# Kernel optimization log

Measured on AMD Instinct MI355X. Metric: run time of the kernel, lower is better.

## Reference

```python
import jax, jax.numpy as jnp
from jax import lax
import numpy as np

NUM_HEADS = 8
ALPHA = 4.0  # spikingjelly default Sigmoid surrogate alpha
TAU = 2.0
BN_EPS = 1e-5

@jax.custom_vjp
def spike(x):
    # Heaviside(v - v_th) with sigmoid surrogate gradient
    return (x >= 0).astype(x.dtype)

def _spike_fwd(x):
    return spike(x), x

def _spike_bwd(x, g):
    sg = jax.nn.sigmoid(ALPHA * x)
    return (g * ALPHA * sg * (1.0 - sg),)

spike.defvjp(_spike_fwd, _spike_bwd)

def lif(x_seq, v_threshold=1.0):
    """Multi-step LIF, tau=2, hard reset to v_reset=0, detach_reset=True.
    x_seq: (T, ...) -> spikes (T, ...)."""
    def step(v, xt):
        h = v + (xt - v) / TAU
        s = spike(h - v_threshold)
        v_next = h * (1.0 - lax.stop_gradient(s))  # detach_reset hard reset
        return v_next, s
    _, s_seq = lax.scan(step, jnp.zeros_like(x_seq[0]), x_seq)
    return s_seq

def bn1d(x, gamma, beta, mean, var):
    # x: (T,B,C,N), normalize over channel dim C (eval-mode BatchNorm1d)
    inv = gamma / jnp.sqrt(var + BN_EPS)
    return x * inv[:, None] + (beta - mean * inv)[:, None]

def setup_inputs() -> dict:
    key = jax.random.key(0)
    ks = jax.random.split(key, 8)
    T, B, C, H, W = 4, 16, 384, 32, 32
    N = H * W
    Dh = C // NUM_HEADS
    x = jax.random.normal(ks[0], (T, B, C, H, W), dtype=jnp.float32)
    attn_k = jax.random.randint(ks[1], (T, B, NUM_HEADS, Dh, N), 0, 2).astype(jnp.bool_)
    attn_v = jax.random.randint(ks[2], (T, B, NUM_HEADS, Dh, N), 0, 2).astype(jnp.bool_)
    wq = jax.random.normal(ks[3], (C, C), dtype=jnp.float32) * 0.02
    wp = jax.random.normal(ks[4], (C, C), dtype=jnp.float32) * 0.02
    bp = jnp.zeros((C,), dtype=jnp.float32)
    return {
        'x': x, 'attn_k': attn_k, 'attn_v': attn_v,
        'wq': wq,
        'q_gamma': jnp.ones((C,), jnp.float32), 'q_beta': jnp.zeros((C,), jnp.float32),
        'q_mean': jnp.zeros((C,), jnp.float32), 'q_var': jnp.ones((C,), jnp.float32),
        'wp': wp, 'bp': bp,
        'p_gamma': jnp.ones((C,), jnp.float32), 'p_beta': jnp.zeros((C,), jnp.float32),
        'p_mean': jnp.zeros((C,), jnp.float32), 'p_var': jnp.ones((C,), jnp.float32),
    }

def reference(x, attn_k, attn_v, wq, q_gamma, q_beta, q_mean, q_var,
              wp, bp, p_gamma, p_beta, p_mean, p_var):
    T, B, C, H, W = x.shape
    N = H * W
    Dh = C // NUM_HEADS
    xs = lif(x).reshape(T, B, C, N)                      # shortcut_lif + flatten(3)
    q = jnp.einsum('oc,tbcn->tbon', wq, xs)              # q_conv (1x1, no bias)
    q = bn1d(q, q_gamma, q_beta, q_mean, q_var)          # q_bn
    q = lif(q)                                           # q_lif
    q = q.reshape(T, B, NUM_HEADS, Dh, N)
    kv = jnp.logical_and(attn_k, attn_v).astype(q.dtype) # attn_k & attn_v
    out = (q * kv).reshape(T, B, C, N)                   # elementwise 'attention'
    out = jnp.einsum('oc,tbcn->tbon', wp, out) + bp[:, None]  # proj_conv (bias)
    out = bn1d(out, p_gamma, p_beta, p_mean, p_var)      # proj_bn
    return out.reshape(T, B, C, H, W)
```

## Files before the change

kernel.cpp:

```cpp
#include <hip/hip_runtime.h>
#include <cstdint>

#define CN (384*1024)
#define BCN (16*CN)
#define EPS 1e-5f

typedef float f32x2 __attribute__((ext_vector_type(2)));
typedef float f32x4 __attribute__((ext_vector_type(4)));

#define WPT_OFF   0u
#define WQB_OFF   589824u
#define QINV_OFF  1179648u
#define QOFF_OFF  (QINV_OFF + 1536u)
#define PINV_OFF  (QINV_OFF + 3072u)
#define POFF_OFF  (QINV_OFF + 4608u)
#define C0_OFF    (QINV_OFF + 6144u)
#define LCNT2_OFF 1187840u
#define ROWMAX_OFF 1253376u
#define MAXQ_OFF  1254912u
#define XM_OFF    1310720u
#define XMT_OFF   4456448u
#define LISTS2_OFF 7602176u
#define ABND_OFF  10747904u
#define MST_OFF   XM_OFF

__global__ __launch_bounds__(256) void k01_lif_prep(const float* __restrict__ x,
                                                    const float* __restrict__ wq,
                                                    const float* __restrict__ wp,
                                                    const float* __restrict__ qg,
                                                    const float* __restrict__ qb,
                                                    const float* __restrict__ qm,
                                                    const float* __restrict__ qv,
                                                    const float* __restrict__ pg,
                                                    const float* __restrict__ pb,
                                                    const float* __restrict__ pm,
                                                    const float* __restrict__ pv,
                                                    const float* __restrict__ bp,
                                                    unsigned long long* __restrict__ xm,
                                                    char* __restrict__ ws) {
    if (blockIdx.x < 1536) {
        const int wv   = threadIdx.x >> 6;
        const int lane = threadIdx.x & 63;
        const int pid  = blockIdx.x * 4 + wv;
        const int b = pid / 384, c = pid % 384;
        const float* xp = x + (size_t)b * CN + (size_t)c * 1024 + lane;
        float v[16];
        #pragma unroll
        for (int g = 0; g < 16; ++g) v[g] = 0.f;
        #pragma unroll
        for (int t = 0; t < 4; ++t) {
            float xv[16];
            #pragma unroll
            for (int g = 0; g < 16; ++g)
                xv[g] = xp[(size_t)t * BCN + g * 64];
            #pragma unroll
            for (int g = 0; g < 16; ++g) {
                float h = v[g] + (xv[g] - v[g]) * 0.5f;
                bool s = (h >= 1.0f);
                unsigned long long m = __ballot(s);
                v[g] = s ? 0.f : h;
                if (lane == 0) xm[(((size_t)t * 16 + b) * 16 + g) * 384 + c] = m;
            }
        }
        return;
    }
    int bid = blockIdx.x - 1536;
    if (bid < 576) {
        int i = bid * 256 + threadIdx.x;
        int c = i / 384, o = i % 384;
        ((float*)(ws + WPT_OFF))[c * 384 + o] = wp[o * 384 + c];
    } else if (bid < 1154) {
        int j = (bid - 576) * 256 + threadIdx.x;
        if (j >= 147840) return;
        int r = j / 384, o = j % 384;
        unsigned short v = 0;
        if (r < 384) {
            unsigned u = __float_as_uint(wq[o * 384 + r]);
            v = (unsigned short)((u + 0x7fffu + ((u >> 16) & 1u)) >> 16);
        }
        ((unsigned short*)(ws + WQB_OFF))[j] = v;
    } else if (bid == 1154) {
        __shared__ float smi[256], smo[256];
        float mi = 0.f, mo = 0.f;
        for (int i = threadIdx.x; i < 384; i += 256) {
            float qi = qg[i] / sqrtf(qv[i] + EPS);
            ((float*)(ws + QINV_OFF))[i] = qi;
            float qov = qb[i] - qm[i] * qi;
            ((float*)(ws + QOFF_OFF))[i] = qov;
            float pi = pg[i] / sqrtf(pv[i] + EPS);
            float po = pb[i] - pm[i] * pi;
            ((float*)(ws + PINV_OFF))[i] = pi;
            ((float*)(ws + POFF_OFF))[i] = po;
            ((float*)(ws + C0_OFF))[i] = bp[i] * pi + po;
            mi = fmaxf(mi, fabsf(qi));
            mo = fmaxf(mo, fabsf(qov));
        }
        smi[threadIdx.x] = mi; smo[threadIdx.x] = mo;
        __syncthreads();
        for (int s = 128; s > 0; s >>= 1) {
            if (threadIdx.x < s) {
                smi[threadIdx.x] = fmaxf(smi[threadIdx.x], smi[threadIdx.x + s]);
                smo[threadIdx.x] = fmaxf(smo[threadIdx.x], smo[threadIdx.x + s]);
            }
            __syncthreads();
        }
        if (threadIdx.x == 0) {
            ((float*)(ws + MAXQ_OFF))[0] = smi[0];
            ((float*)(ws + MAXQ_OFF))[1] = smo[0];
        }
    } else {
        __shared__ float sm[256];
        int rblk = bid - 1155;
        int row = rblk * 64 + (threadIdx.x >> 2);
        int qd  = threadIdx.x & 3;
        float m = 0.f;
        for (int o = qd * 96; o < qd * 96 + 96; ++o) {
            unsigned u = __float_as_uint(wq[(size_t)o * 384 + row]);
            unsigned bbits = (u + 0x7fffu + ((u >> 16) & 1u)) >> 16;
            m = fmaxf(m, __uint_as_float((bbits & 0x7fffu) << 16));
        }
        sm[threadIdx.x] = m;
        __syncthreads();
        if (qd == 0) {
            float r0 = fmaxf(fmaxf(sm[threadIdx.x], sm[threadIdx.x + 1]),
                             fmaxf(sm[threadIdx.x + 2], sm[threadIdx.x + 3]));
            ((float*)(ws + ROWMAX_OFF))[row] = r0;
        }
    }
}

__global__ __launch_bounds__(256) void k1bc(const unsigned long long* __restrict__ xm,
                                            const float* __restrict__ rowmaxp,
                                            const float* __restrict__ maxqp,
                                            unsigned long long* __restrict__ xmT,
                                            unsigned short* __restrict__ lists2,
                                            unsigned char* __restrict__ lcnt2,
                                            unsigned char* __restrict__ abnd) {
    int wid  = (blockIdx.x * 256 + threadIdx.x) >> 6;
    int lane = threadIdx.x & 63;
    int g  = wid & 15;
    int tb = wid >> 4;
    unsigned long long T[6];
    #pragma unroll
    for (int cg = 0; cg < 6; ++cg) {
        unsigned long long W = xm[((size_t)tb * 16 + g) * 384 + cg * 64 + lane];
        unsigned long long colw = 0ull;
        #pragma unroll
        for (int k = 0; k < 64; ++k) {
            unsigned long long bk = __ballot((W >> k) & 1ull);
            if (lane == k) colw = bk;
        }
        T[cg] = colw;
    }
    const int n   = g * 64 + lane;
    const size_t col = ((size_t)tb << 10) + n;
    #pragma unroll
    for (int cg = 0; cg < 6; ++cg) xmT[col * 6 + cg] = T[cg];
    const int blockid = (tb & 15) * 64 + (n >> 4);
    const int un = (n & 15) * 4 + (tb >> 4);
    unsigned short* lp = lists2 + ((size_t)blockid * 64 + un) * 24;
    int k = 0;
    float S = 0.f;
    #pragma unroll
    for (int cg = 0; cg < 6; ++cg) {
        unsigned long long m = T[cg];
        while (m) {
            int j = __builtin_ctzll(m);
            m &= m - 1;
            S += rowmaxp[cg * 64 + j];
            if (k < 24) lp[k] = (unsigned short)((cg * 64 + j) * 3);
            ++k;
        }
    }
    int kk = k > 24 ? 24 : k;
    for (int i = kk; i < 24; ++i) lp[i] = 1152;
    lcnt2[(size_t)blockid * 64 + un] =
        (k > 24) ? 0xFF : (unsigned char)((k + 7) >> 3);
    float A = maxqp[0] * S + maxqp[1];
    int aq = (int)ceilf(A * 64.f);
    abnd[(size_t)blockid * 64 + un] = (unsigned char)(aq > 255 ? 255 : (aq < 0 ? 0 : aq));
}

#define BLO(w) __uint_as_float((w) << 16)
#define BHI(w) __uint_as_float((w) & 0xFFFF0000u)
#define PK(w)  ((f32x2){BLO(w), BHI(w)})
#define RL(v, l) ((unsigned)__builtin_amdgcn_readlane((int)(v), (l)))

#define GROW8(W0, W1, W2, W3) do {                                                \
    uint3 d0_ = *(const uint3*)(wqc + ((size_t)((W0) & 0xffffu) << 8) + voff);    \
    uint3 d1_ = *(const uint3*)(wqc + ((size_t)((W0) >> 16) << 8) + voff);        \
    uint3 d2_ = *(const uint3*)(wqc + ((size_t)((W1) & 0xffffu) << 8) + voff);    \
    uint3 d3_ = *(const uint3*)(wqc + ((size_t)((W1) >> 16) << 8) + voff);        \
    uint3 d4_ = *(const uint3*)(wqc + ((size_t)((W2) & 0xffffu) << 8) + voff);    \
    uint3 d5_ = *(const uint3*)(wqc + ((size_t)((W2) >> 16) << 8) + voff);        \
    uint3 d6_ = *(const uint3*)(wqc + ((size_t)((W3) & 0xffffu) << 8) + voff);    \
    uint3 d7_ = *(const uint3*)(wqc + ((size_t)((W3) >> 16) << 8) + voff);        \
    s0 += ((PK(d0_.x) + PK(d1_.x)) + (PK(d2_.x) + PK(d3_.x)))                     \
        + ((PK(d4_.x) + PK(d5_.x)) + (PK(d6_.x) + PK(d7_.x)));                    \
    s1 += ((PK(d0_.y) + PK(d1_.y)) + (PK(d2_.y) + PK(d3_.y)))                     \
        + ((PK(d4_.y) + PK(d5_.y)) + (PK(d6_.y) + PK(d7_.y)));                    \
    s2 += ((PK(d0_.z) + PK(d1_.z)) + (PK(d2_.z) + PK(d3_.z)))                     \
        + ((PK(d4_.z) + PK(d5_.z)) + (PK(d6_.z) + PK(d7_.z)));                    \
} while (0)

__global__ __launch_bounds__(512) void k2_qpath(const char* __restrict__ wqc,
                                                const float* __restrict__ qinv_,
                                                const float* __restrict__ qoff_,
                                                const unsigned short* __restrict__ lists2,
                                                const unsigned char* __restrict__ lcnt2,
                                                const unsigned char* __restrict__ abnd,
                                                const unsigned long long* __restrict__ xmT,
                                                const unsigned char* __restrict__ ak,
                                                const unsigned char* __restrict__ av,
                                                const float* __restrict__ c0,
                                                unsigned long long* __restrict__ msT,
                                                float* __restrict__ out) {
    const int tid  = threadIdx.x;
    const int lane = tid & 63;
    const int w    = tid >> 6;
    const int nt   = blockIdx.x & 63;
    const int b    = blockIdx.x >> 6;
    const int voff = lane * 12;

    const char* lb = (const char*)lists2 + (size_t)blockIdx.x * 3072 + lane * 48;
    const uint4 L0 = *(const uint4*)lb;
    const uint4 L1 = *(const uint4*)(lb + 16);
    const uint4 L2 = *(const uint4*)(lb + 32);
    const unsigned lcv = *(const unsigned*)((const char*)lcnt2
                          + (size_t)blockIdx.x * 64 + (lane & 15) * 4);
    const unsigned abv = *(const unsigned*)((const char*)abnd
                          + (size_t)blockIdx.x * 64 + (lane & 15) * 4);

    float qi[6], qo[6];
    #pragma unroll
    for (int e = 0; e < 6; ++e) {
        qi[e] = qinv_[lane * 6 + e];
        qo[e] = qoff_[lane * 6 + e];
    }

    #pragma unroll
    for (int i = 0; i < 2; ++i) {
        const int nl = w * 2 + i;
        const int n  = nt * 16 + nl;
        const unsigned abw = RL(abv, nl);
        float hb = 0.f;
        bool skip = true;
        #pragma unroll
        for (int t = 0; t < 4; ++t) {
            float A = (float)((abw >> (8 * t)) & 0xffu) * 0.015625f + 0.015625f;
            hb = 0.5f * (hb + A);
            skip = skip && (hb < 1.0f);
        }
        if (skip) {
            if (lane < 6) {
                #pragma unroll
                for (int t = 0; t < 4; ++t)
                    msT[(size_t)(((t * 16 + b) << 10) + n) * 6 + lane] = 0ull;
            }
            continue;
        }
        const unsigned lcw = RL(lcv, nl);
        float v[6] = {0.f, 0.f, 0.f, 0.f, 0.f, 0.f};
        #pragma unroll
        for (int t = 0; t < 4; ++t) {
            const int un = nl * 4 + t;
            const unsigned r_ = (lcw >> (8 * t)) & 0xffu;
            f32x2 s0 = {0.f, 0.f}, s1 = {0.f, 0.f}, s2 = {0.f, 0.f};
            {
                const unsigned Wa = RL(L0.x, un), Wb = RL(L0.y, un);
                const unsigned Wc = RL(L0.z, un), Wd = RL(L0.w, un);
                const unsigned We = RL(L1.x, un), Wf = RL(L1.y, un);
                const unsigned Wg = RL(L1.z, un), Wh = RL(L1.w, un);
                GROW8(Wa, Wb, Wc, Wd);
                GROW8(We, Wf, Wg, Wh);
            }
            if (r_ == 3u) {
                const unsigned Wa = RL(L2.x, un), Wb = RL(L2.y, un);
                const unsigned Wc = RL(L2.z, un), Wd = RL(L2.w, un);
                GROW8(Wa, Wb, Wc, Wd);
            }
            if (r_ == 0xffu) {
                const int colf = ((t * 16 + b) << 10) + n;
                const unsigned long long* mp = xmT + (size_t)colf * 6;
                s0 = (f32x2){0.f, 0.f}; s1 = (f32x2){0.f, 0.f}; s2 = (f32x2){0.f, 0.f};
                #pragma unroll
                for (int cg = 0; cg < 6; ++cg) {
                    unsigned long long mm = mp[cg];
                    while (mm) {
                        int j = __builtin_ctzll(mm);
                        mm &= mm - 1;
                        uint3 dd = *(const uint3*)(wqc + (size_t)(cg * 64 + j) * 768 + voff);
                        s0 += PK(dd.x); s1 += PK(dd.y); s2 += PK(dd.z);
                    }
                }
            }
            const int col = ((t * 16 + b) << 10) + n;
            const float val[6] = {s0.x, s0.y, s1.x, s1.y, s2.x, s2.y};
            bool sp[6];
            #pragma unroll
            for (int e = 0; e < 6; ++e) {
                float q = val[e] * qi[e] + qo[e];
                float h = 0.5f * (v[e] + q);
                bool s = (h >= 1.0f);
                v[e] = s ? 0.f : h;
                if (s) {
                    size_t ix = ((size_t)((t * 16 + b) * 384 + lane * 6 + e) << 10) + n;
                    s = (ak[ix] != 0) && (av[ix] != 0);
                }
                sp[e] = s;
            }
            unsigned long long B0 = __ballot(sp[0]);
            unsigned long long B1 = __ballot(sp[1]);
            unsigned long long B2 = __ballot(sp[2]);
            unsigned long long B3 = __ballot(sp[3]);
            unsigned long long B4 = __ballot(sp[4]);
            unsigned long long B5 = __ballot(sp[5]);
            unsigned long long sel = lane == 0 ? B0 : lane == 1 ? B1 : lane == 2 ? B2
                                   : lane == 3 ? B3 : lane == 4 ? B4 : B5;
            if (lane < 6) msT[(size_t)col * 6 + lane] = sel;
        }
    }

    {
        float cv[3];
        #pragma unroll
        for (int k = 0; k < 3; ++k) cv[k] = c0[(tid + k * 512) >> 2];
        #pragma unroll
        for (int t = 0; t < 4; ++t) {
            f32x4* base4 = (f32x4*)out + (size_t)(t * 16 + b) * 384 * 256 + nt * 4;
            #pragma unroll
            for (int k = 0; k < 3; ++k) {
                int i2 = tid + k * 512;
                int o = i2 >> 2, n4 = i2 & 3;
                float vv = cv[k];
                __builtin_nontemporal_store((f32x4){vv, vv, vv, vv},
                                            base4 + (size_t)o * 256 + n4);
            }
        }
    }
}

__global__ __launch_bounds__(384) void k3_proj(const float* __restrict__ wpT,
                                               const float* __restrict__ pinv_,
                                               const float* __restrict__ poff_,
                                               const float* __restrict__ bp,
                                               const unsigned long long* __restrict__ msT,
                                               float* __restrict__ out) {
    __shared__ unsigned int wflag[6];
    const int tid = threadIdx.x;
    const int bid = blockIdx.x;
    const int g = bid & 15, b = (bid >> 4) & 15, t = bid >> 8;
    const unsigned long long* mbase = msT + ((size_t)(t * 16 + b) * 1024 + g * 64) * 6;
    unsigned long long m = mbase[tid];
    unsigned long long anyb = __ballot(m != 0ull);
    if ((tid & 63) == 0) wflag[tid >> 6] = (anyb != 0ull) ? 1u : 0u;
    __syncthreads();
    unsigned int any = wflag[0] | wflag[1] | wflag[2] | wflag[3] | wflag[4] | wflag[5];
    if (!any) return;

    size_t obase = (size_t)(t * 16 + b) * 384;
    float pi = pinv_[tid], po = poff_[tid], bb = bp[tid];
    for (int nl = 0; nl < 64; ++nl) {
        float acc = 0.f;
        #pragma unroll
        for (int u = 0; u < 6; ++u) {
            unsigned long long mm = mbase[nl * 6 + u];
            while (mm) {
                int j = __builtin_ctzll(mm);
                mm &= mm - 1;
                int row = j * 6 + u;
                acc += wpT[(size_t)row * 384 + tid];
            }
        }
        out[(obase + tid) * 1024 + g * 64 + nl] = (acc + bb) * pi + po;
    }
}

extern "C" void kernel_launch(void* const* d_in, const int* in_sizes, int n_in,
                              void* d_out, int out_size, void* d_ws, size_t ws_size,
                              hipStream_t stream) {
    const float* x  = (const float*)d_in[0];
    const unsigned char* ak = (const unsigned char*)d_in[1];
    const unsigned char* av = (const unsigned char*)d_in[2];
    const float* wq = (const float*)d_in[3];
    const float* qg = (const float*)d_in[4];
    const float* qb = (const float*)d_in[5];
    const float* qm = (const float*)d_in[6];
    const float* qv = (const float*)d_in[7];
    const float* wp = (const float*)d_in[8];
    const float* bp = (const float*)d_in[9];
    const float* pg = (const float*)d_in[10];
    const float* pb = (const float*)d_in[11];
    const float* pm = (const float*)d_in[12];
    const float* pv = (const float*)d_in[13];
    char* ws = (char*)d_ws;
    float* out = (float*)d_out;

    hipLaunchKernelGGL(k01_lif_prep, dim3(2697), dim3(256), 0, stream,
                       x, wq, wp, qg, qb, qm, qv, pg, pb, pm, pv, bp,
                       (unsigned long long*)(ws + XM_OFF), ws);
    hipLaunchKernelGGL(k1bc, dim3(256), dim3(256), 0, stream,
                       (const unsigned long long*)(ws + XM_OFF),
                       (const float*)(ws + ROWMAX_OFF),
                       (const float*)(ws + MAXQ_OFF),
                       (unsigned long long*)(ws + XMT_OFF),
                       (unsigned short*)(ws + LISTS2_OFF),
                       (unsigned char*)(ws + LCNT2_OFF),
                       (unsigned char*)(ws + ABND_OFF));
    hipLaunchKernelGGL(k2_qpath, dim3(1024), dim3(512), 0, stream,
                       (const char*)(ws + WQB_OFF),
                       (const float*)(ws + QINV_OFF), (const float*)(ws + QOFF_OFF),
                       (const unsigned short*)(ws + LISTS2_OFF),
                       (const unsigned char*)(ws + LCNT2_OFF),
                       (const unsigned char*)(ws + ABND_OFF),
                       (const unsigned long long*)(ws + XMT_OFF), ak, av,
                       (const float*)(ws + C0_OFF),
                       (unsigned long long*)(ws + MST_OFF), out);
    hipLaunchKernelGGL(k3_proj, dim3(1024), dim3(384), 0, stream,
                       (const float*)(ws + WPT_OFF), (const float*)(ws + PINV_OFF),
                       (const float*)(ws + POFF_OFF), bp,
                       (const unsigned long long*)(ws + MST_OFF), out);
}
```

Baseline: 86.81 us.

## Move constant output prefill into prep kernel and coalesce weight transposes

The bias-constant fill of the whole output tensor moves out of the q-path kernel into extra blocks of the first prep kernel, which compute the per-channel constant on the fly. It can then run alongside the LIF blocks instead of adding store traffic to the compute-heavy q-path kernel. The weight transpose and bf16 conversion loops now read coalesced and scatter their writes, and the row-max reduction is reorganised across waves. The prep kernel gets more blocks and writes the full output, which may lengthen that stage.

```diff
diff --git a/kernel.cpp b/kernel.cpp
--- a/kernel.cpp
+++ b/kernel.cpp
@@ -14,7 +14,6 @@
 #define QOFF_OFF  (QINV_OFF + 1536u)
 #define PINV_OFF  (QINV_OFF + 3072u)
 #define POFF_OFF  (QINV_OFF + 4608u)
-#define C0_OFF    (QINV_OFF + 6144u)
 #define LCNT2_OFF 1187840u
 #define ROWMAX_OFF 1253376u
 #define MAXQ_OFF  1254912u
@@ -37,7 +36,8 @@
                                                     const float* __restrict__ pv,
                                                     const float* __restrict__ bp,
                                                     unsigned long long* __restrict__ xm,
-                                                    char* __restrict__ ws) {
+                                                    char* __restrict__ ws,
+                                                    float* __restrict__ out) {
     if (blockIdx.x < 1536) {
         const int wv   = threadIdx.x >> 6;
         const int lane = threadIdx.x & 63;
@@ -64,22 +64,40 @@
         }
         return;
     }
-    int bid = blockIdx.x - 1536;
-    if (bid < 576) {
-        int i = bid * 256 + threadIdx.x;
-        int c = i / 384, o = i % 384;
+    if (blockIdx.x < 3072) {
+        __shared__ float sc0[16];
+        const int w2 = blockIdx.x - 1536;
+        if (threadIdx.x < 16) {
+            int o = (w2 * 16 + threadIdx.x) % 384;
+            float pi = pg[o] / sqrtf(pv[o] + EPS);
+            float po = pb[o] - pm[o] * pi;
+            sc0[threadIdx.x] = bp[o] * pi + po;
+        }
+        __syncthreads();
+        f32x4* ob = (f32x4*)out + (size_t)w2 * 4096;
+        #pragma unroll
+        for (int k = 0; k < 16; ++k) {
+            float vv = sc0[k];
+            __builtin_nontemporal_store((f32x4){vv, vv, vv, vv},
+                                        ob + k * 256 + threadIdx.x);
+        }
+        return;
+    }
+    if (blockIdx.x < 3648) {
+        int i = (blockIdx.x - 3072) * 256 + threadIdx.x;
+        int o = i / 384, c = i % 384;
         ((float*)(ws + WPT_OFF))[c * 384 + o] = wp[o * 384 + c];
-    } else if (bid < 1154) {
-        int j = (bid - 576) * 256 + threadIdx.x;
-        if (j >= 147840) return;
-        int r = j / 384, o = j % 384;
-        unsigned short v = 0;
-        if (r < 384) {
-            unsigned u = __float_as_uint(wq[o * 384 + r]);
-            v = (unsigned short)((u + 0x7fffu + ((u >> 16) & 1u)) >> 16);
-        }
-        ((unsigned short*)(ws + WQB_OFF))[j] = v;
-    } else if (bid == 1154) {
+        return;
+    }
+    if (blockIdx.x < 4224) {
+        int j = (blockIdx.x - 3648) * 256 + threadIdx.x;
+        int o = j / 384, r = j % 384;
+        unsigned u = __float_as_uint(wq[o * 384 + r]);
+        unsigned short v = (unsigned short)((u + 0x7fffu + ((u >> 16) & 1u)) >> 16);
+        ((unsigned short*)(ws + WQB_OFF))[r * 384 + o] = v;
+        return;
+    }
+    if (blockIdx.x == 4224) {
         __shared__ float smi[256], smo[256];
         float mi = 0.f, mo = 0.f;
         for (int i = threadIdx.x; i < 384; i += 256) {
@@ -88,10 +106,9 @@
             float qov = qb[i] - qm[i] * qi;
             ((float*)(ws + QOFF_OFF))[i] = qov;
             float pi = pg[i] / sqrtf(pv[i] + EPS);
-            float po = pb[i] - pm[i] * pi;
             ((float*)(ws + PINV_OFF))[i] = pi;
-            ((float*)(ws + POFF_OFF))[i] = po;
-            ((float*)(ws + C0_OFF))[i] = bp[i] * pi + po;
+            ((float*)(ws + POFF_OFF))[i] = pb[i] - pm[i] * pi;
+            ((unsigned short*)(ws + WQB_OFF))[384 * 384 + i] = 0;
             mi = fmaxf(mi, fabsf(qi));
             mo = fmaxf(mo, fabsf(qov));
         }
@@ -108,23 +125,26 @@
             ((float*)(ws + MAXQ_OFF))[0] = smi[0];
             ((float*)(ws + MAXQ_OFF))[1] = smo[0];
         }
-    } else {
-        __shared__ float sm[256];
-        int rblk = bid - 1155;
-        int row = rblk * 64 + (threadIdx.x >> 2);
-        int qd  = threadIdx.x & 3;
+        return;
+    }
+    {
+        __shared__ float sm2[4][64];
+        const int rb = blockIdx.x - 4225;
+        const int lane = threadIdx.x & 63;
+        const int wv = threadIdx.x >> 6;
+        const int r = rb * 64 + lane;
         float m = 0.f;
-        for (int o = qd * 96; o < qd * 96 + 96; ++o) {
-            unsigned u = __float_as_uint(wq[(size_t)o * 384 + row]);
+        for (int o = wv * 96; o < wv * 96 + 96; ++o) {
+            unsigned u = __float_as_uint(wq[(size_t)o * 384 + r]);
             unsigned bbits = (u + 0x7fffu + ((u >> 16) & 1u)) >> 16;
             m = fmaxf(m, __uint_as_float((bbits & 0x7fffu) << 16));
         }
-        sm[threadIdx.x] = m;
+        sm2[wv][lane] = m;
         __syncthreads();
-        if (qd == 0) {
-            float r0 = fmaxf(fmaxf(sm[threadIdx.x], sm[threadIdx.x + 1]),
-                             fmaxf(sm[threadIdx.x + 2], sm[threadIdx.x + 3]));
-            ((float*)(ws + ROWMAX_OFF))[row] = r0;
+        if (wv == 0) {
+            float r0 = fmaxf(fmaxf(sm2[0][lane], sm2[1][lane]),
+                             fmaxf(sm2[2][lane], sm2[3][lane]));
+            ((float*)(ws + ROWMAX_OFF))[r] = r0;
         }
     }
 }
@@ -212,9 +232,7 @@
                                                 const unsigned long long* __restrict__ xmT,
                                                 const unsigned char* __restrict__ ak,
                                                 const unsigned char* __restrict__ av,
-                                                const float* __restrict__ c0,
-                                                unsigned long long* __restrict__ msT,
-                                                float* __restrict__ out) {
+                                                unsigned long long* __restrict__ msT) {
     const int tid  = threadIdx.x;
     const int lane = tid & 63;
     const int w    = tid >> 6;
@@ -318,24 +336,6 @@
             unsigned long long sel = lane == 0 ? B0 : lane == 1 ? B1 : lane == 2 ? B2
                                    : lane == 3 ? B3 : lane == 4 ? B4 : B5;
             if (lane < 6) msT[(size_t)col * 6 + lane] = sel;
-        }
-    }
-
-    {
-        float cv[3];
-        #pragma unroll
-        for (int k = 0; k < 3; ++k) cv[k] = c0[(tid + k * 512) >> 2];
-        #pragma unroll
-        for (int t = 0; t < 4; ++t) {
-            f32x4* base4 = (f32x4*)out + (size_t)(t * 16 + b) * 384 * 256 + nt * 4;
-            #pragma unroll
-            for (int k = 0; k < 3; ++k) {
-                int i2 = tid + k * 512;
-                int o = i2 >> 2, n4 = i2 & 3;
-                float vv = cv[k];
-                __builtin_nontemporal_store((f32x4){vv, vv, vv, vv},
-                                            base4 + (size_t)o * 256 + n4);
-            }
         }
     }
 }
@@ -396,9 +396,9 @@
     char* ws = (char*)d_ws;
     float* out = (float*)d_out;
 
-    hipLaunchKernelGGL(k01_lif_prep, dim3(2697), dim3(256), 0, stream,
+    hipLaunchKernelGGL(k01_lif_prep, dim3(4231), dim3(256), 0, stream,
                        x, wq, wp, qg, qb, qm, qv, pg, pb, pm, pv, bp,
-                       (unsigned long long*)(ws + XM_OFF), ws);
+                       (unsigned long long*)(ws + XM_OFF), ws, out);
     hipLaunchKernelGGL(k1bc, dim3(256), dim3(256), 0, stream,
                        (const unsigned long long*)(ws + XM_OFF),
                        (const float*)(ws + ROWMAX_OFF),
@@ -414,8 +414,7 @@
                        (const unsigned char*)(ws + LCNT2_OFF),
                        (const unsigned char*)(ws + ABND_OFF),
                        (const unsigned long long*)(ws + XMT_OFF), ak, av,
-                       (const float*)(ws + C0_OFF),
-                       (unsigned long long*)(ws + MST_OFF), out);
+                       (unsigned long long*)(ws + MST_OFF));
     hipLaunchKernelGGL(k3_proj, dim3(1024), dim3(384), 0, stream,
                        (const float*)(ws + WPT_OFF), (const float*)(ws + PINV_OFF),
                        (const float*)(ws + POFF_OFF), bp,
```

Result: no change. 86.41 us (-0.5%).
